# Kernel tuning notes

Hardware: AMD Instinct MI355X
Metric: run time of the kernel (lower is better)

## Reference

```python
import jax, jax.numpy as jnp
import numpy as np

B, N, DIM, HEADS = 4, 1024, 1024, 16
DH = DIM // HEADS
SCALE = 1.0 / np.sqrt(DH)
EPS = 1e-6


def clinear(x, Wr, Wi, br, bi):
    # (a+bi)(Wr+Wi i): real = a Wr^T - b Wi^T, imag = a Wi^T + b Wr^T
    xr, xi = x.real, x.imag
    real = xr @ Wr.T - xi @ Wi.T + br
    imag = xr @ Wi.T + xi @ Wr.T + bi
    return jax.lax.complex(real, imag)


def cln(x, gamma, beta):
    # normalize magnitude over last dim, keep phase
    mag = jnp.abs(x)
    phase = jnp.angle(x)
    mean = jnp.mean(mag, axis=-1, keepdims=True)
    var = jnp.var(mag, axis=-1, keepdims=True)
    nm = (mag - mean) / jnp.sqrt(var + EPS)
    nm = nm * gamma + beta
    return jax.lax.complex(nm * jnp.cos(phase), nm * jnp.sin(phase))


def forward(xr, xi, Wq_r, Wq_i, bq_r, bq_i, Wk_r, Wk_i, bk_r, bk_i,
            Wv_r, Wv_i, bv_r, bv_i, Wo_r, Wo_i, bo_r, bo_i,
            gq, beq, gk, bek, gv, bev):
    x = jax.lax.complex(xr, xi)  # [B,N,D] complex64

    def heads(t):
        return t.reshape(B, N, HEADS, DH).transpose(0, 2, 1, 3)  # [B,H,N,dh]

    Q = heads(cln(clinear(x, Wq_r, Wq_i, bq_r, bq_i), gq, beq))
    K = heads(cln(clinear(x, Wk_r, Wk_i, bk_r, bk_i), gk, bek))
    V = heads(cln(clinear(x, Wv_r, Wv_i, bv_r, bv_i), gv, bev))

    Qf = jnp.fft.fft(Q, axis=2, norm='ortho')
    Kf = jnp.fft.fft(K, axis=2, norm='ortho')
    Vf = jnp.fft.fft(V, axis=2, norm='ortho')

    scores = jnp.einsum('bhnd,bhmd->bhnm', Qf, jnp.conj(Kf)) * SCALE
    attn = jax.nn.softmax(scores.real, axis=-1)  # real-valued softmax
    # attn is real; multiply into complex Vf componentwise
    out_f = jax.lax.complex(jnp.einsum('bhnm,bhmd->bhnd', attn, Vf.real),
                            jnp.einsum('bhnm,bhmd->bhnd', attn, Vf.imag))
    out = jnp.fft.ifft(out_f, axis=2, norm='ortho')
    out = out.transpose(0, 2, 1, 3).reshape(B, N, DIM)
    y = clinear(out, Wo_r, Wo_i, bo_r, bo_i)
    # return real||imag concatenated on last axis (float32 view of complex output)
    return jnp.concatenate([y.real, y.imag], axis=-1)


def setup_inputs() -> dict:
    key = jax.random.key(0)
    ks = jax.random.split(key, 16)
    wscale = np.sqrt(2.0 / (DIM + DIM)).astype(np.float32)
    d = {}
    d['xr'] = jax.random.normal(ks[0], (B, N, DIM), jnp.float32)
    d['xi'] = jax.random.normal(ks[1], (B, N, DIM), jnp.float32)
    i = 2
    for name in ('q', 'k', 'v', 'o'):
        d[f'W{name}_r'] = jax.random.normal(ks[i], (DIM, DIM), jnp.float32) * wscale; i += 1
        d[f'W{name}_i'] = jax.random.normal(ks[i], (DIM, DIM), jnp.float32) * wscale; i += 1
        d[f'b{name}_r'] = jnp.zeros((DIM,), jnp.float32)
        d[f'b{name}_i'] = jnp.zeros((DIM,), jnp.float32)
    for name in ('q', 'k', 'v'):
        d[f'g{name}'] = jnp.ones((DIM,), jnp.float32)
        d[f'be{name}'] = jnp.zeros((DIM,), jnp.float32)
    return d


def reference(xr, xi, Wq_r, Wq_i, bq_r, bq_i, Wk_r, Wk_i, bk_r, bk_i,
              Wv_r, Wv_i, bv_r, bv_i, Wo_r, Wo_i, bo_r, bo_i,
              gq, beq, gk, bek, gv, bev):
    return forward(xr, xi, Wq_r, Wq_i, bq_r, bq_i, Wk_r, Wk_i, bk_r, bk_i,
                   Wv_r, Wv_i, bv_r, bv_i, Wo_r, Wo_i, bo_r, bo_i,
                   gq, beq, gk, bek, gv, bev)
```

## Files before the change

### kernel.cpp

```cpp
#include <hip/hip_runtime.h>
#include <math.h>

#define BB 4
#define NN 1024
#define DIMM 1024
#define HHH 16
#define DHH 64
#define BN 4096
#define EPS_LN 1e-6f

typedef __bf16 bf16_t;
typedef __bf16 bf16x8 __attribute__((ext_vector_type(8)));
typedef __bf16 bf16x4 __attribute__((ext_vector_type(4)));
typedef float f32x4 __attribute__((ext_vector_type(4)));
typedef float f32x16 __attribute__((ext_vector_type(16)));
#define MFMA16(a, b, c) __builtin_amdgcn_mfma_f32_16x16x32_bf16(a, b, c, 0, 0, 0)
#define MFMA32(a, b, c) __builtin_amdgcn_mfma_f32_32x32x16_bf16(a, b, c, 0, 0, 0)
#define AS1 __attribute__((address_space(1)))
#define AS3 __attribute__((address_space(3)))

__device__ inline unsigned pk2(float a, float b) {
  union { bf16_t h[2]; unsigned u; } c;
  c.h[0] = (bf16_t)a; c.h[1] = (bf16_t)b;
  return c.u;
}
union U16 { uint4 u; bf16x8 v; };

__global__ __launch_bounds__(256) void pack_x(
    const float* __restrict__ xr, const float* __restrict__ xi,
    bf16_t* __restrict__ out)
{
  int t = blockIdx.x * 256 + threadIdx.x;
  size_t e = (size_t)t * 8;
  int row = (int)(e >> 11), col = (int)(e & 2047);
  const float* src = (col < 1024) ? (xr + (size_t)row * 1024 + col)
                                  : (xi + (size_t)row * 1024 + col - 1024);
  float4 a = *(const float4*)src;
  float4 b = *(const float4*)(src + 4);
  bf16x8 o;
  o[0] = (bf16_t)a.x; o[1] = (bf16_t)a.y; o[2] = (bf16_t)a.z; o[3] = (bf16_t)a.w;
  o[4] = (bf16_t)b.x; o[5] = (bf16_t)b.y; o[6] = (bf16_t)b.z; o[7] = (bf16_t)b.w;
  *(bf16x8*)(out + e) = o;
}

__global__ __launch_bounds__(256) void pack_w(
    const float* __restrict__ Wr, const float* __restrict__ Wi,
    const float* __restrict__ br, const float* __restrict__ bi,
    bf16_t* __restrict__ Wcat, float* __restrict__ bcat)
{
  int t = blockIdx.x * 256 + threadIdx.x;
  size_t e = (size_t)t * 8;
  int row = (int)(e >> 11), col = (int)(e & 2047);
  const float* src;
  float sgn = 1.f;
  if (row < 1024) {
    if (col < 1024) src = Wr + (size_t)row * 1024 + col;
    else          { src = Wi + (size_t)row * 1024 + col - 1024; sgn = -1.f; }
  } else {
    int r2 = row - 1024;
    if (col < 1024) src = Wi + (size_t)r2 * 1024 + col;
    else            src = Wr + (size_t)r2 * 1024 + col - 1024;
  }
  float4 a = *(const float4*)src;
  float4 b = *(const float4*)(src + 4);
  bf16x8 o;
  o[0] = (bf16_t)(sgn * a.x); o[1] = (bf16_t)(sgn * a.y);
  o[2] = (bf16_t)(sgn * a.z); o[3] = (bf16_t)(sgn * a.w);
  o[4] = (bf16_t)(sgn * b.x); o[5] = (bf16_t)(sgn * b.y);
  o[6] = (bf16_t)(sgn * b.z); o[7] = (bf16_t)(sgn * b.w);
  *(bf16x8*)(Wcat + e) = o;
  if (e < 2048) {
#pragma unroll
    for (int j = 0; j < 8; ++j) {
      int n = (int)e + j;
      bcat[n] = (n < 1024) ? br[n] : bi[n - 1024];
    }
  }
}

__global__ __launch_bounds__(256) void gemm_qkv(
    const bf16_t* __restrict__ A, const bf16_t* __restrict__ Bt,
    const float* __restrict__ bias, bf16_t* __restrict__ C6)
{
  __shared__ bf16_t sA[2][128 * 64];
  __shared__ bf16_t sB[2][128 * 64];
  const int tid = threadIdx.x;
  const int w = tid >> 6, l = tid & 63;
  const int lo4 = l & 15, hi = l >> 4;
  const int wr = w >> 1, wc = w & 1;
  const int row0 = blockIdx.y * 128, col0 = blockIdx.x * 128;

  const int srow = (l >> 3);
  const int scol = (l & 7) * 8;
  const bf16_t* gA[4];
  const bf16_t* gB[4];
#pragma unroll
  for (int i = 0; i < 4; ++i) {
    int r = (w * 4 + i) * 8 + srow;
    gA[i] = A  + (size_t)(row0 + r) * 2048 + scol;
    gB[i] = Bt + (size_t)(col0 + r) * 2048 + scol;
  }

  f32x4 acc[4][4] = {};
  const int nk = 2048 / 64;
#pragma unroll
  for (int i = 0; i < 4; ++i) {
    __builtin_amdgcn_global_load_lds((const AS1 void*)(gA[i]),
                                     (AS3 void*)&sA[0][(w * 4 + i) * 512], 16, 0, 0);
    __builtin_amdgcn_global_load_lds((const AS1 void*)(gB[i]),
                                     (AS3 void*)&sB[0][(w * 4 + i) * 512], 16, 0, 0);
  }
#pragma unroll
  for (int i = 0; i < 4; ++i) {
    __builtin_amdgcn_global_load_lds((const AS1 void*)(gA[i] + 64),
                                     (AS3 void*)&sA[1][(w * 4 + i) * 512], 16, 0, 0);
    __builtin_amdgcn_global_load_lds((const AS1 void*)(gB[i] + 64),
                                     (AS3 void*)&sB[1][(w * 4 + i) * 512], 16, 0, 0);
  }
  for (int t = 0; t < nk; ++t) {
    const int ct = t & 1;
    if (t + 1 < nk) asm volatile("s_waitcnt vmcnt(8)" ::: "memory");
    else            asm volatile("s_waitcnt vmcnt(0)" ::: "memory");
    __builtin_amdgcn_sched_barrier(0);
    __builtin_amdgcn_s_barrier();
    __builtin_amdgcn_sched_barrier(0);
#pragma unroll
    for (int kk = 0; kk < 2; ++kk) {
      bf16x8 am[4], bn[4];
#pragma unroll
      for (int i = 0; i < 4; ++i)
        am[i] = *(const bf16x8*)&sA[ct][(wr * 64 + i * 16 + lo4) * 64 + kk * 32 + hi * 8];
#pragma unroll
      for (int j = 0; j < 4; ++j)
        bn[j] = *(const bf16x8*)&sB[ct][(wc * 64 + j * 16 + lo4) * 64 + kk * 32 + hi * 8];
#pragma unroll
      for (int i = 0; i < 4; ++i)
#pragma unroll
        for (int j = 0; j < 4; ++j)
          acc[i][j] = MFMA16(am[i], bn[j], acc[i][j]);
    }
    __builtin_amdgcn_s_barrier();
    __builtin_amdgcn_sched_barrier(0);
    if (t + 2 < nk) {
      int k2 = (t + 2) * 64;
#pragma unroll
      for (int i = 0; i < 4; ++i) {
        __builtin_amdgcn_global_load_lds((const AS1 void*)(gA[i] + k2),
                                         (AS3 void*)&sA[ct][(w * 4 + i) * 512], 16, 0, 0);
        __builtin_amdgcn_global_load_lds((const AS1 void*)(gB[i] + k2),
                                         (AS3 void*)&sB[ct][(w * 4 + i) * 512], 16, 0, 0);
      }
    }
  }
  const int colg0 = col0 + wc * 64;
#pragma unroll
  for (int i = 0; i < 4; ++i) {
#pragma unroll
    for (int j = 0; j < 4; ++j) {
      float bv = bias[colg0 + j * 16 + lo4];
#pragma unroll
      for (int r = 0; r < 4; ++r) {
        int rowg = row0 + wr * 64 + i * 16 + hi * 4 + r;
        C6[(size_t)rowg * 6144 + colg0 + j * 16 + lo4] = (bf16_t)(acc[i][j][r] + bv);
      }
    }
  }
}

__global__ __launch_bounds__(256) void gemm_bf16(
    const bf16_t* __restrict__ A, const bf16_t* __restrict__ Bt,
    const float* __restrict__ bias,
    float* __restrict__ Cr, float* __restrict__ Ci, int ldc)
{
  __shared__ bf16_t sA[2][128 * 64];
  __shared__ bf16_t sB[2][128 * 64];
  const int tid = threadIdx.x;
  const int w = tid >> 6, l = tid & 63;
  const int lo4 = l & 15, hi = l >> 4;
  const int wr = w >> 1, wc = w & 1;
  const int row0 = blockIdx.y * 128, col0 = blockIdx.x * 128;

  const int srow = (l >> 3);
  const int scol = (l & 7) * 8;
  const bf16_t* gA[4];
  const bf16_t* gB[4];
#pragma unroll
  for (int i = 0; i < 4; ++i) {
    int r = (w * 4 + i) * 8 + srow;
    gA[i] = A  + (size_t)(row0 + r) * 2048 + scol;
    gB[i] = Bt + (size_t)(col0 + r) * 2048 + scol;
  }

  f32x4 acc[4][4] = {};
  const int nk = 2048 / 64;
#pragma unroll
  for (int i = 0; i < 4; ++i) {
    __builtin_amdgcn_global_load_lds((const AS1 void*)(gA[i]),
                                     (AS3 void*)&sA[0][(w * 4 + i) * 512], 16, 0, 0);
    __builtin_amdgcn_global_load_lds((const AS1 void*)(gB[i]),
                                     (AS3 void*)&sB[0][(w * 4 + i) * 512], 16, 0, 0);
  }
#pragma unroll
  for (int i = 0; i < 4; ++i) {
    __builtin_amdgcn_global_load_lds((const AS1 void*)(gA[i] + 64),
                                     (AS3 void*)&sA[1][(w * 4 + i) * 512], 16, 0, 0);
    __builtin_amdgcn_global_load_lds((const AS1 void*)(gB[i] + 64),
                                     (AS3 void*)&sB[1][(w * 4 + i) * 512], 16, 0, 0);
  }
  for (int t = 0; t < nk; ++t) {
    const int ct = t & 1;
    if (t + 1 < nk) asm volatile("s_waitcnt vmcnt(8)" ::: "memory");
    else            asm volatile("s_waitcnt vmcnt(0)" ::: "memory");
    __builtin_amdgcn_sched_barrier(0);
    __builtin_amdgcn_s_barrier();
    __builtin_amdgcn_sched_barrier(0);
#pragma unroll
    for (int kk = 0; kk < 2; ++kk) {
      bf16x8 am[4], bn[4];
#pragma unroll
      for (int i = 0; i < 4; ++i)
        am[i] = *(const bf16x8*)&sA[ct][(wr * 64 + i * 16 + lo4) * 64 + kk * 32 + hi * 8];
#pragma unroll
      for (int j = 0; j < 4; ++j)
        bn[j] = *(const bf16x8*)&sB[ct][(wc * 64 + j * 16 + lo4) * 64 + kk * 32 + hi * 8];
#pragma unroll
      for (int i = 0; i < 4; ++i)
#pragma unroll
        for (int j = 0; j < 4; ++j)
          acc[i][j] = MFMA16(am[i], bn[j], acc[i][j]);
    }
    __builtin_amdgcn_s_barrier();
    __builtin_amdgcn_sched_barrier(0);
    if (t + 2 < nk) {
      int k2 = (t + 2) * 64;
#pragma unroll
      for (int i = 0; i < 4; ++i) {
        __builtin_amdgcn_global_load_lds((const AS1 void*)(gA[i] + k2),
                                         (AS3 void*)&sA[ct][(w * 4 + i) * 512], 16, 0, 0);
        __builtin_amdgcn_global_load_lds((const AS1 void*)(gB[i] + k2),
                                         (AS3 void*)&sB[ct][(w * 4 + i) * 512], 16, 0, 0);
      }
    }
  }
  const int colg0 = col0 + wc * 64;
  float* Cp = (colg0 < 1024) ? Cr : Ci;
  const int cb = colg0 & 1023;
#pragma unroll
  for (int i = 0; i < 4; ++i) {
#pragma unroll
    for (int j = 0; j < 4; ++j) {
      float bv = bias[colg0 + j * 16 + lo4];
#pragma unroll
      for (int r = 0; r < 4; ++r) {
        int rowg = row0 + wr * 64 + i * 16 + hi * 4 + r;
        Cp[(size_t)rowg * ldc + cb + j * 16 + lo4] = acc[i][j][r] + bv;
      }
    }
  }
}

__global__ __launch_bounds__(256) void ln_stats3(
    const bf16_t* __restrict__ C6, float2* __restrict__ st)
{
  __shared__ float red[8];
  const int row = blockIdx.x;
  const int p = blockIdx.y;
  const int tid = threadIdx.x;
  const bf16_t* pr = C6 + (size_t)row * 6144 + p * 2048;
  const bf16_t* pi = pr + 1024;
  bf16x4 vr = *(const bf16x4*)(pr + tid * 4);
  bf16x4 vi = *(const bf16x4*)(pi + tid * 4);
  float s = 0.f, s2 = 0.f;
#pragma unroll
  for (int t = 0; t < 4; ++t) {
    float a = (float)vr[t], b = (float)vi[t];
    float mg = sqrtf(a * a + b * b);
    s += mg; s2 += mg * mg;
  }
#pragma unroll
  for (int o = 32; o; o >>= 1) { s += __shfl_down(s, o); s2 += __shfl_down(s2, o); }
  if ((tid & 63) == 0) { red[tid >> 6] = s; red[4 + (tid >> 6)] = s2; }
  __syncthreads();
  if (tid == 0) {
    float S = red[0] + red[1] + red[2] + red[3];
    float S2 = red[4] + red[5] + red[6] + red[7];
    float mean = S * (1.f / DIMM);
    float var = S2 * (1.f / DIMM) - mean * mean;
    st[(size_t)p * 4096 + row] = make_float2(mean, rsqrtf(var + EPS_LN));
  }
}

#define LIDX(d_, c_) (((d_) << 10) + ((c_) ^ (((c_) >> 5) & 31) ^ (((d_) & 7) << 2)))

__global__ __launch_bounds__(512) void fft_kernel(
    const bf16_t* __restrict__ inR, const bf16_t* __restrict__ inI,
    bf16_t* __restrict__ outR, bf16_t* __restrict__ outI,
    int in_sb, int in_sh, int in_sn, int in_sd,
    int out_sb, int out_sh, int out_sn,
    float sign, float oscale, int imode, int omode,
    const float2* __restrict__ stats,
    const float* __restrict__ gamma, const float* __restrict__ beta)
{
  __shared__ float lr[8 * 1024], li[8 * 1024];
  __shared__ float2 tw[1024];
  const int tid = threadIdx.x;
  const int dc = blockIdx.x & 7;
  const int bh = blockIdx.x >> 3;
  const int b = bh >> 4, h = bh & 15;
  const bf16_t* bR = inR + (size_t)b * in_sb + (size_t)h * in_sh;
  const bf16_t* bI = inI + (size_t)b * in_sb + (size_t)h * in_sh;
#pragma unroll
  for (int t = tid; t < 1024; t += 512) {
    float ang = sign * 3.14159265358979323846f * (float)t * (1.f / 512.f);
    float sn, cs;
    __sincosf(ang, &sn, &cs);
    tw[t] = make_float2(cs, sn);
  }
  if (imode == 0) {
    float gg[8], bb[8];
    if (stats) {
#pragma unroll
      for (int ds = 0; ds < 8; ++ds) {
        gg[ds] = gamma[h * DHH + dc * 8 + ds];
        bb[ds] = beta[h * DHH + dc * 8 + ds];
      }
    }
#pragma unroll
    for (int rep = 0; rep < 2; ++rep) {
      int n = tid + rep * 512;
      bf16x8 r8 = *(const bf16x8*)(bR + (size_t)n * in_sn + dc * 8);
      bf16x8 i8 = *(const bf16x8*)(bI + (size_t)n * in_sn + dc * 8);
      float ur[8], ui[8];
#pragma unroll
      for (int ds = 0; ds < 8; ++ds) { ur[ds] = (float)r8[ds]; ui[ds] = (float)i8[ds]; }
      if (stats) {
        float2 stv = stats[b * NN + n];
#pragma unroll
        for (int ds = 0; ds < 8; ++ds) {
          float a = ur[ds], c2 = ui[ds];
          float mag = sqrtf(a * a + c2 * c2);
          float nm = (mag - stv.x) * stv.y * gg[ds] + bb[ds];
          if (mag > 0.f) { float sc = nm / mag; ur[ds] = a * sc; ui[ds] = c2 * sc; }
          else           { ur[ds] = nm; ui[ds] = 0.f; }
        }
      }
#pragma unroll
      for (int ds = 0; ds < 8; ++ds) {
        int ax = LIDX(ds, n);
        lr[ax] = ur[ds];
        li[ax] = ui[ds];
      }
    }
  } else {
    const int ds = tid & 7, nb = tid >> 3;
    const bf16_t* pR = bR + (size_t)(dc * 8 + ds) * in_sd + nb * 16;
    const bf16_t* pI = bI + (size_t)(dc * 8 + ds) * in_sd + nb * 16;
    bf16x8 a0 = *(const bf16x8*)pR, a1 = *(const bf16x8*)(pR + 8);
    bf16x8 b0 = *(const bf16x8*)pI, b1 = *(const bf16x8*)(pI + 8);
#pragma unroll
    for (int k = 0; k < 8; ++k) {
      int c = nb * 16 + k;
      lr[LIDX(ds, c)] = (float)a0[k];       li[LIDX(ds, c)] = (float)b0[k];
      lr[LIDX(ds, c + 8)] = (float)a1[k];   li[LIDX(ds, c + 8)] = (float)b1[k];
    }
  }
  __syncthreads();
  const int dsub = tid & 7;
  const int jb = tid >> 3;
  int lq2 = 8;
  for (int st = 0; st < 5; ++st) {
    const int qtr = 1 << lq2;
    const int tmul = 1 << (2 * st);
    for (int jt = 0; jt < 4; ++jt) {
      int j = jb + jt * 64;
      int o = j & (qtr - 1);
      int i0 = ((j >> lq2) << (lq2 + 2)) + o;
      int a0 = LIDX(dsub, i0);
      int a1 = LIDX(dsub, i0 + qtr);
      int a2 = LIDX(dsub, i0 + 2 * qtr);
      int a3 = LIDX(dsub, i0 + 3 * qtr);
      float x0r = lr[a0], x0i = li[a0];
      float x1r = lr[a1], x1i = li[a1];
      float x2r = lr[a2], x2i = li[a2];
      float x3r = lr[a3], x3i = li[a3];
      float ar = x0r + x2r, ai2 = x0i + x2i;
      float br = x0r - x2r, bi  = x0i - x2i;
      float cr = x1r + x3r, ci  = x1i + x3i;
      float dr = x1r - x3r, di  = x1i - x3i;
      float2 t1 = tw[o * tmul];
      float2 t2 = tw[2 * o * tmul];
      float2 t3 = tw[3 * o * tmul];
      lr[a0] = ar + cr;  li[a0] = ai2 + ci;
      float u1r = br - sign * di, u1i = bi + sign * dr;
      lr[a1] = u1r * t1.x - u1i * t1.y;  li[a1] = u1r * t1.y + u1i * t1.x;
      float u2r = ar - cr, u2i = ai2 - ci;
      lr[a2] = u2r * t2.x - u2i * t2.y;  li[a2] = u2r * t2.y + u2i * t2.x;
      float u3r = br + sign * di, u3i = bi - sign * dr;
      lr[a3] = u3r * t3.x - u3i * t3.y;  li[a3] = u3r * t3.y + u3i * t3.x;
    }
    __syncthreads();
    lq2 -= 2;
  }
  bf16_t* oRb = outR + (size_t)b * out_sb + (size_t)h * out_sh;
  bf16_t* oIb = outI + (size_t)b * out_sb + (size_t)h * out_sh;
#pragma unroll
  for (int rep = 0; rep < 2; ++rep) {
    int n = tid + rep * 512;
    int rv2 = __brev((unsigned)n) >> 22;
    int p = ((rv2 & 0x155) << 1) | ((rv2 >> 1) & 0x155);
    float fr[8], fi[8];
#pragma unroll
    for (int ds = 0; ds < 8; ++ds) {
      fr[ds] = lr[LIDX(ds, p)] * oscale;
      fi[ds] = li[LIDX(ds, p)] * oscale;
    }
    if (omode == 1) {
      size_t tb = (size_t)(n >> 5) * 4096;
#pragma unroll
      for (int ds = 0; ds < 8; ++ds) {
        int dch = dc * 8 + ds;
        size_t ga = tb + (size_t)dch * 32 + ((n & 31) ^ (((dch >> 1) & 3) << 3));
        oRb[ga] = (bf16_t)fr[ds];
        oIb[ga] = (bf16_t)fi[ds];
      }
    } else {
      int cb = dc * 8;
      if (omode == 2) cb = (dc ^ (n & 7)) * 8;
      bf16x8 v0, w0;
#pragma unroll
      for (int k = 0; k < 8; ++k) {
        v0[k] = (bf16_t)fr[k];
        w0[k] = (bf16_t)fi[k];
      }
      size_t gb = (size_t)n * out_sn + cb;
      *(bf16x8*)(oRb + gb) = v0;
      *(bf16x8*)(oIb + gb) = w0;
    }
  }
}

__global__ __launch_bounds__(256, 2) void fattn(
    const bf16_t* __restrict__ Qf, const bf16_t* __restrict__ Kfs,
    const bf16_t* __restrict__ Vfs, bf16_t* __restrict__ OT)
{
  __shared__ bf16_t K3[3][4096];
  __shared__ bf16_t V3[3][4096];
  const int tid = threadIdx.x;
  const int w = tid >> 6, l = tid & 63;
  const int lq = l & 31;
  const int h = l >> 5;
  const int i = blockIdx.x;
  const int j = i >> 3;
  const int bh = (i & 7) * 8 + (j >> 3);
  const int q0 = (j & 7) * 128 + w * 32;

  bf16x8 bq[8];
  const bf16_t* qp = Qf + ((size_t)bh * NN + q0 + lq) * 128 + h * 8;
#pragma unroll
  for (int kk = 0; kk < 8; ++kk) bq[kk] = *(const bf16x8*)(qp + kk * 16);

  f32x16 o[4] = {};
  float m = -3e38f, ln = 0.f;

  const bf16_t* kg = Kfs + (size_t)bh * 131072 + w * 1024 + l * 8;
  const bf16_t* vg = Vfs + (size_t)bh * 131072 + w * 1024 + l * 8;
  const int kswz = (lq & 7) << 3;
  const int vswz = ((lq >> 1) & 3) << 3;

#pragma unroll
  for (int tt = 0; tt < 2; ++tt) {
    const bf16_t* kt = kg + (size_t)tt * 4096;
    const bf16_t* vt = vg + (size_t)tt * 4096;
#pragma unroll
    for (int ii = 0; ii < 2; ++ii) {
      __builtin_amdgcn_global_load_lds((const AS1 void*)(kt + ii * 512),
                                       (AS3 void*)&K3[tt][w * 1024 + ii * 512], 16, 0, 0);
      __builtin_amdgcn_global_load_lds((const AS1 void*)(vt + ii * 512),
                                       (AS3 void*)&V3[tt][w * 1024 + ii * 512], 16, 0, 0);
    }
  }
  asm volatile("s_waitcnt vmcnt(4)" ::: "memory");
  __builtin_amdgcn_s_barrier();
  __builtin_amdgcn_sched_barrier(0);

  int cur = 0;
  for (int t = 0; t < 32; ++t) {
    if (t < 30) {
      int nb = cur + 2; if (nb >= 3) nb -= 3;
      const bf16_t* kt = kg + (size_t)(t + 2) * 4096;
      const bf16_t* vt = vg + (size_t)(t + 2) * 4096;
#pragma unroll
      for (int ii = 0; ii < 2; ++ii) {
        __builtin_amdgcn_global_load_lds((const AS1 void*)(kt + ii * 512),
                                         (AS3 void*)&K3[nb][w * 1024 + ii * 512], 16, 0, 0);
        __builtin_amdgcn_global_load_lds((const AS1 void*)(vt + ii * 512),
                                         (AS3 void*)&V3[nb][w * 1024 + ii * 512], 16, 0, 0);
      }
    }

    f32x16 s = {};
#pragma unroll
    for (int kk = 0; kk < 8; ++kk) {
      bf16x8 ak = *(const bf16x8*)&K3[cur][lq * 128 + ((kk * 16 + h * 8) ^ kswz)];
      s = MFMA32(ak, bq[kk], s);
    }

    float pmax = s[0];
#pragma unroll
    for (int r = 1; r < 16; ++r) pmax = fmaxf(pmax, s[r]);
    pmax = fmaxf(pmax, __shfl_xor(pmax, 32));
    if (!__all(pmax - m <= 8.f)) {
      float mnew = fmaxf(m, pmax);
      float alpha = __expf(m - mnew);
      m = mnew;
      ln *= alpha;
#pragma unroll
      for (int db = 0; db < 4; ++db)
#pragma unroll
        for (int r = 0; r < 16; ++r) o[db][r] *= alpha;
    }
    float pf[16];
    float rs = 0.f;
#pragma unroll
    for (int r = 0; r < 16; ++r) { pf[r] = __expf(s[r] - m); rs += pf[r]; }
    rs += __shfl_xor(rs, 32);
    ln += rs;

    unsigned pw[8];
#pragma unroll
    for (int ii = 0; ii < 8; ++ii) pw[ii] = pk2(pf[2 * ii], pf[2 * ii + 1]);
    unsigned r0 = (unsigned)__shfl_xor((int)(h ? pw[0] : pw[2]), 32);
    unsigned r1 = (unsigned)__shfl_xor((int)(h ? pw[1] : pw[3]), 32);
    unsigned r2 = (unsigned)__shfl_xor((int)(h ? pw[4] : pw[6]), 32);
    unsigned r3 = (unsigned)__shfl_xor((int)(h ? pw[5] : pw[7]), 32);
    U16 bp0, bp1;
    bp0.u.x = h ? r0 : pw[0];  bp0.u.y = h ? r1 : pw[1];
    bp0.u.z = h ? pw[2] : r0;  bp0.u.w = h ? pw[3] : r1;
    bp1.u.x = h ? r2 : pw[4];  bp1.u.y = h ? r3 : pw[5];
    bp1.u.z = h ? pw[6] : r2;  bp1.u.w = h ? pw[7] : r3;

#pragma unroll
    for (int db = 0; db < 4; ++db) {
      int r = db * 32 + lq;
      bf16x8 av0 = *(const bf16x8*)&V3[cur][r * 32 + ((h * 8) ^ vswz)];
      bf16x8 av1 = *(const bf16x8*)&V3[cur][r * 32 + ((16 + h * 8) ^ vswz)];
      o[db] = MFMA32(av0, bp0.v, o[db]);
      o[db] = MFMA32(av1, bp1.v, o[db]);
    }

    if (t < 31) {
      if (t < 30) asm volatile("s_waitcnt vmcnt(4)" ::: "memory");
      else        asm volatile("s_waitcnt vmcnt(0)" ::: "memory");
      __builtin_amdgcn_s_barrier();
      __builtin_amdgcn_sched_barrier(0);
    }
    cur = (cur == 2) ? 0 : cur + 1;
  }

  float inv = 1.f / ln;
  const size_t otb = (size_t)bh * 128 * NN + q0 + lq;
#pragma unroll
  for (int db = 0; db < 4; ++db)
#pragma unroll
    for (int r = 0; r < 16; ++r) {
      int dl = (r & 3) + 8 * (r >> 2) + 4 * h;
      OT[otb + (size_t)(db * 32 + dl) * NN] = (bf16_t)(o[db][r] * inv);
    }
}

extern "C" void kernel_launch(void* const* d_in, const int* in_sizes, int n_in,
                              void* d_out, int out_size, void* d_ws, size_t ws_size,
                              hipStream_t stream) {
  const float* xr   = (const float*)d_in[0];
  const float* xi   = (const float*)d_in[1];
  const float* Wqr  = (const float*)d_in[2];
  const float* Wqi  = (const float*)d_in[3];
  const float* bqr  = (const float*)d_in[4];
  const float* bqi  = (const float*)d_in[5];
  const float* Wkr  = (const float*)d_in[6];
  const float* Wki  = (const float*)d_in[7];
  const float* bkr  = (const float*)d_in[8];
  const float* bki  = (const float*)d_in[9];
  const float* Wvr  = (const float*)d_in[10];
  const float* Wvi  = (const float*)d_in[11];
  const float* bvr  = (const float*)d_in[12];
  const float* bvi  = (const float*)d_in[13];
  const float* Wor  = (const float*)d_in[14];
  const float* Woi  = (const float*)d_in[15];
  const float* bor  = (const float*)d_in[16];
  const float* boi  = (const float*)d_in[17];
  const float* gq   = (const float*)d_in[18];
  const float* beq  = (const float*)d_in[19];
  const float* gk   = (const float*)d_in[20];
  const float* bek  = (const float*)d_in[21];
  const float* gv   = (const float*)d_in[22];
  const float* bev  = (const float*)d_in[23];

  char* wp = (char*)d_ws;
  bf16_t* Axaug = (bf16_t*)wp;  wp += (size_t)4096 * 2048 * 2;
  bf16_t* Wcat3 = (bf16_t*)wp;  wp += (size_t)6144 * 2048 * 2;
  float*  bcat3 = (float*)wp;   wp += (size_t)6144 * 4;
  float2* lnst3 = (float2*)wp;  wp += (size_t)3 * 4096 * 8;
  bf16_t* C6    = (bf16_t*)wp;  wp += (size_t)4096 * 6144 * 2;
  bf16_t* Qf    = (bf16_t*)wp;  wp += (size_t)64 * 1024 * 128 * 2;
  bf16_t* Kf    = (bf16_t*)wp;  wp += (size_t)64 * 1024 * 128 * 2;
  bf16_t* VfT   = (bf16_t*)wp;  wp += (size_t)64 * 1024 * 128 * 2;
  bf16_t* OT    = C6;
  bf16_t* Yaug  = Qf;

  const dim3 gQKV(48, 32);
  const dim3 gGemmO(16, 32);
  const int gPackX = (4096 * 2048 / 8) / 256;
  const int gPackW = (2048 * 2048 / 8) / 256;
  const dim3 gLn(4096, 3);
  const int gFft = 64 * 8;
  const int gAtt = 64 * 8;

  pack_x<<<gPackX, 256, 0, stream>>>(xr, xi, Axaug);
  pack_w<<<gPackW, 256, 0, stream>>>(Wqr, Wqi, bqr, bqi,
                                     Wcat3, bcat3);
  pack_w<<<gPackW, 256, 0, stream>>>(Wkr, Wki, bkr, bki,
                                     Wcat3 + (size_t)2048 * 2048, bcat3 + 2048);
  pack_w<<<gPackW, 256, 0, stream>>>(Wvr, Wvi, bvr, bvi,
                                     Wcat3 + (size_t)4096 * 2048, bcat3 + 4096);

  gemm_qkv<<<gQKV, 256, 0, stream>>>(Axaug, Wcat3, bcat3, C6);
  ln_stats3<<<gLn, 256, 0, stream>>>(C6, lnst3);

  fft_kernel<<<gFft, 512, 0, stream>>>(C6, C6 + 1024, Qf, Qf + 64,
      NN * 6144, DHH, 6144, 1,
      16 * NN * 128, NN * 128, 128,
      -1.0f, 0.03125f * 0.125f, 0, 0, lnst3, gq, beq);
  fft_kernel<<<gFft, 512, 0, stream>>>(C6 + 2048, C6 + 3072, Kf, Kf + 64,
      NN * 6144, DHH, 6144, 1,
      16 * NN * 128, NN * 128, 128,
      -1.0f, 0.03125f, 0, 2, lnst3 + 4096, gk, bek);
  fft_kernel<<<gFft, 512, 0, stream>>>(C6 + 4096, C6 + 5120, VfT, VfT + 2048,
      NN * 6144, DHH, 6144, 1,
      16 * 131072, 131072, 0,
      -1.0f, 0.03125f, 0, 1, lnst3 + 8192, gv, bev);

  fattn<<<gAtt, 256, 0, stream>>>(Qf, Kf, VfT, OT);

  fft_kernel<<<gFft, 512, 0, stream>>>(OT, OT + (size_t)64 * NN, Yaug, Yaug + 1024,
      16 * 128 * NN, 128 * NN, 1, NN,
      NN * 2048, 64, 2048,
      +1.0f, 0.03125f, 1, 0, nullptr, nullptr, nullptr);

  float* yout = (float*)d_out;
  pack_w<<<gPackW, 256, 0, stream>>>(Wor, Woi, bor, boi, Wcat3, bcat3);
  gemm_bf16<<<gGemmO, 256, 0, stream>>>(Yaug, Wcat3, bcat3, yout, yout + 1024, 2048);
}
```

Baseline: 402.6 us.

## Retile QKV GEMM to 256x256 blocks with 4-stage swizzled LDS pipeline

The QKV projection GEMM moves from 128x128 tiles with 256 threads and double buffering to 256x256 tiles with 512 threads (8 waves, each computing 128x64). It uses a 4-deep ring of K=32 LDS stages with an XOR swizzle on columns to avoid bank conflicts, and raises wave priority around the MFMA bursts. The larger tile doubles operand reuse and cuts global traffic per FLOP. The cost is a grid of only 384 blocks, which risks poor occupancy and tail balance on a 256-CU part, plus more registers for accumulators.

```diff
diff --git a/kernel.cpp b/kernel.cpp
--- a/kernel.cpp
+++ b/kernel.cpp
@@ -78,93 +78,88 @@
   }
 }
 
-__global__ __launch_bounds__(256) void gemm_qkv(
+__global__ __launch_bounds__(512, 2) void gemm_qkv(
     const bf16_t* __restrict__ A, const bf16_t* __restrict__ Bt,
     const float* __restrict__ bias, bf16_t* __restrict__ C6)
 {
-  __shared__ bf16_t sA[2][128 * 64];
-  __shared__ bf16_t sB[2][128 * 64];
+  __shared__ bf16_t sA[4][8192];
+  __shared__ bf16_t sB[4][8192];
   const int tid = threadIdx.x;
   const int w = tid >> 6, l = tid & 63;
   const int lo4 = l & 15, hi = l >> 4;
-  const int wr = w >> 1, wc = w & 1;
-  const int row0 = blockIdx.y * 128, col0 = blockIdx.x * 128;
-
-  const int srow = (l >> 3);
-  const int scol = (l & 7) * 8;
-  const bf16_t* gA[4];
-  const bf16_t* gB[4];
-#pragma unroll
-  for (int i = 0; i < 4; ++i) {
-    int r = (w * 4 + i) * 8 + srow;
-    gA[i] = A  + (size_t)(row0 + r) * 2048 + scol;
-    gB[i] = Bt + (size_t)(col0 + r) * 2048 + scol;
-  }
-
-  f32x4 acc[4][4] = {};
-  const int nk = 2048 / 64;
-#pragma unroll
-  for (int i = 0; i < 4; ++i) {
-    __builtin_amdgcn_global_load_lds((const AS1 void*)(gA[i]),
-                                     (AS3 void*)&sA[0][(w * 4 + i) * 512], 16, 0, 0);
-    __builtin_amdgcn_global_load_lds((const AS1 void*)(gB[i]),
-                                     (AS3 void*)&sB[0][(w * 4 + i) * 512], 16, 0, 0);
-  }
-#pragma unroll
-  for (int i = 0; i < 4; ++i) {
-    __builtin_amdgcn_global_load_lds((const AS1 void*)(gA[i] + 64),
-                                     (AS3 void*)&sA[1][(w * 4 + i) * 512], 16, 0, 0);
-    __builtin_amdgcn_global_load_lds((const AS1 void*)(gB[i] + 64),
-                                     (AS3 void*)&sB[1][(w * 4 + i) * 512], 16, 0, 0);
-  }
-  for (int t = 0; t < nk; ++t) {
-    const int ct = t & 1;
-    if (t + 1 < nk) asm volatile("s_waitcnt vmcnt(8)" ::: "memory");
-    else            asm volatile("s_waitcnt vmcnt(0)" ::: "memory");
+  const int wm = w >> 2, wn = w & 3;
+  const int row0 = blockIdx.y * 256, col0 = blockIdx.x * 256;
+
+  const int sr = tid >> 2;
+  const int sc = ((tid & 3) * 8) ^ ((sr & 3) << 3);
+  const bf16_t* gA0 = A  + (size_t)(row0 + sr) * 2048 + sc;
+  const bf16_t* gA1 = A  + (size_t)(row0 + 128 + sr) * 2048 + sc;
+  const bf16_t* gB0 = Bt + (size_t)(col0 + sr) * 2048 + sc;
+  const bf16_t* gB1 = Bt + (size_t)(col0 + 128 + sr) * 2048 + sc;
+
+#define STAGE256(tt, b) {                                                        \
+    int k0_ = (tt) * 32;                                                         \
+    __builtin_amdgcn_global_load_lds((const AS1 void*)(gA0 + k0_),               \
+        (AS3 void*)&sA[b][tid * 8], 16, 0, 0);                                   \
+    __builtin_amdgcn_global_load_lds((const AS1 void*)(gA1 + k0_),               \
+        (AS3 void*)&sA[b][4096 + tid * 8], 16, 0, 0);                            \
+    __builtin_amdgcn_global_load_lds((const AS1 void*)(gB0 + k0_),               \
+        (AS3 void*)&sB[b][tid * 8], 16, 0, 0);                                   \
+    __builtin_amdgcn_global_load_lds((const AS1 void*)(gB1 + k0_),               \
+        (AS3 void*)&sB[b][4096 + tid * 8], 16, 0, 0); }
+
+  const int rsw = (lo4 & 3) << 3;
+  const int acol = (hi * 8) ^ rsw;
+
+  f32x4 acc[8][4] = {};
+  STAGE256(0, 0);
+  STAGE256(1, 1);
+  STAGE256(2, 2);
+
+  for (int t = 0; t < 64; ++t) {
+    const int buf = t & 3;
+    if (t < 62)       asm volatile("s_waitcnt vmcnt(8)" ::: "memory");
+    else if (t == 62) asm volatile("s_waitcnt vmcnt(4)" ::: "memory");
+    else              asm volatile("s_waitcnt vmcnt(0)" ::: "memory");
     __builtin_amdgcn_sched_barrier(0);
     __builtin_amdgcn_s_barrier();
     __builtin_amdgcn_sched_barrier(0);
-#pragma unroll
-    for (int kk = 0; kk < 2; ++kk) {
-      bf16x8 am[4], bn[4];
-#pragma unroll
-      for (int i = 0; i < 4; ++i)
-        am[i] = *(const bf16x8*)&sA[ct][(wr * 64 + i * 16 + lo4) * 64 + kk * 32 + hi * 8];
-#pragma unroll
-      for (int j = 0; j < 4; ++j)
-        bn[j] = *(const bf16x8*)&sB[ct][(wc * 64 + j * 16 + lo4) * 64 + kk * 32 + hi * 8];
-#pragma unroll
-      for (int i = 0; i < 4; ++i)
-#pragma unroll
-        for (int j = 0; j < 4; ++j)
-          acc[i][j] = MFMA16(am[i], bn[j], acc[i][j]);
-    }
-    __builtin_amdgcn_s_barrier();
-    __builtin_amdgcn_sched_barrier(0);
-    if (t + 2 < nk) {
-      int k2 = (t + 2) * 64;
-#pragma unroll
-      for (int i = 0; i < 4; ++i) {
-        __builtin_amdgcn_global_load_lds((const AS1 void*)(gA[i] + k2),
-                                         (AS3 void*)&sA[ct][(w * 4 + i) * 512], 16, 0, 0);
-        __builtin_amdgcn_global_load_lds((const AS1 void*)(gB[i] + k2),
-                                         (AS3 void*)&sB[ct][(w * 4 + i) * 512], 16, 0, 0);
-      }
-    }
-  }
-  const int colg0 = col0 + wc * 64;
-#pragma unroll
-  for (int i = 0; i < 4; ++i) {
-#pragma unroll
-    for (int j = 0; j < 4; ++j) {
-      float bv = bias[colg0 + j * 16 + lo4];
+    if (t + 3 < 64) STAGE256(t + 3, (t + 3) & 3);
+
+    bf16x8 bn[4];
+#pragma unroll
+    for (int nf = 0; nf < 4; ++nf)
+      bn[nf] = *(const bf16x8*)&sB[buf][(wn * 64 + nf * 16 + lo4) * 32 + acol];
+#pragma unroll
+    for (int q = 0; q < 2; ++q) {
+      bf16x8 am[4];
+#pragma unroll
+      for (int mm = 0; mm < 4; ++mm)
+        am[mm] = *(const bf16x8*)&sA[buf][(wm * 128 + (q * 4 + mm) * 16 + lo4) * 32 + acol];
+      __builtin_amdgcn_s_setprio(1);
+#pragma unroll
+      for (int mm = 0; mm < 4; ++mm)
+#pragma unroll
+        for (int nf = 0; nf < 4; ++nf)
+          acc[q * 4 + mm][nf] = MFMA16(am[mm], bn[nf], acc[q * 4 + mm][nf]);
+      __builtin_amdgcn_s_setprio(0);
+    }
+  }
+
+#pragma unroll
+  for (int mi = 0; mi < 8; ++mi) {
+#pragma unroll
+    for (int nf = 0; nf < 4; ++nf) {
+      int colg = col0 + wn * 64 + nf * 16 + lo4;
+      float bv = bias[colg];
 #pragma unroll
       for (int r = 0; r < 4; ++r) {
-        int rowg = row0 + wr * 64 + i * 16 + hi * 4 + r;
-        C6[(size_t)rowg * 6144 + colg0 + j * 16 + lo4] = (bf16_t)(acc[i][j][r] + bv);
-      }
-    }
-  }
+        int rowg = row0 + wm * 128 + mi * 16 + hi * 4 + r;
+        C6[(size_t)rowg * 6144 + colg] = (bf16_t)(acc[mi][nf][r] + bv);
+      }
+    }
+  }
+#undef STAGE256
 }
 
 __global__ __launch_bounds__(256) void gemm_bf16(
@@ -608,7 +603,7 @@
   bf16_t* OT    = C6;
   bf16_t* Yaug  = Qf;
 
-  const dim3 gQKV(48, 32);
+  const dim3 gQKV(24, 16);
   const dim3 gGemmO(16, 32);
   const int gPackX = (4096 * 2048 / 8) / 256;
   const int gPackW = (2048 * 2048 / 8) / 256;
@@ -624,7 +619,7 @@
   pack_w<<<gPackW, 256, 0, stream>>>(Wvr, Wvi, bvr, bvi,
                                      Wcat3 + (size_t)4096 * 2048, bcat3 + 4096);
 
-  gemm_qkv<<<gQKV, 256, 0, stream>>>(Axaug, Wcat3, bcat3, C6);
+  gemm_qkv<<<gQKV, 512, 0, stream>>>(Axaug, Wcat3, bcat3, C6);
   ln_stats3<<<gLn, 256, 0, stream>>>(C6, lnst3);
 
   fft_kernel<<<gFft, 512, 0, stream>>>(C6, C6 + 1024, Qf, Qf + 64,
```

After: 426.7 us. 6.0% more time.
